# Kernel optimization log

Measured on AMD Instinct MI355X. Metric: run time of the kernel, lower is better.

The kernel has to match this reference:

```python
import jax, jax.numpy as jnp
import numpy as np

S = 128          # shared sequence length of v/q/a/k
D = 512          # model dim
H = 8            # n_heads
W = D // H       # head width (becomes the v/q/a einsum axes)
NUM = S // 8     # num_v = num_q = num_a = num_k
SCALE = float(np.sqrt(H))  # source divides by sqrt(a.size(-1)) == sqrt(n_heads)


def _heads(x):
    # split_last(x,(H,-1)).transpose(1,2) on a 2D (S,D) tensor -> (S, W, H)
    return x.reshape(S, H, W).transpose(0, 2, 1)


def setup_inputs() -> dict:
    key = jax.random.key(0)
    ks = jax.random.split(key, 24)
    d = {}
    for i, n in enumerate(['v', 'q', 'a', 'k']):
        d[n] = jax.random.normal(ks[i], (S, D), jnp.float32)
    for n in ['v_mask', 'q_mask', 'a_mask', 'k_mask']:
        d[n] = jnp.ones((S,), jnp.bool_)
    wnames = ['Wv', 'Wq', 'Wa', 'Wk', 'Wvo', 'Wqo', 'Wao', 'Wko']
    bnames = ['bv', 'bq', 'ba', 'bk', 'bvo', 'bqo', 'bao', 'bko']
    for i, (wn, bn) in enumerate(zip(wnames, bnames)):
        d[wn] = jax.random.normal(ks[4 + 2 * i], (D, D), jnp.float32) / np.sqrt(D)
        d[bn] = jax.random.normal(ks[5 + 2 * i], (D,), jnp.float32) * 0.01
    return d


def reference(v, q, a, k, v_mask, q_mask, a_mask, k_mask,
              Wv, bv, Wq, bq, Wa, ba, Wk, bk,
              Wvo, bvo, Wqo, bqo, Wao, bao, Wko, bko):
    # input projections (torch Linear: x @ W.T + b)
    vp = v @ Wv.T + bv
    qp = q @ Wq.T + bq
    ap = a @ Wa.T + ba
    kp = k @ Wk.T + bk
    # output projections are applied to the already-projected tensors
    vo = vp @ Wvo.T + bvo
    qo = qp @ Wqo.T + bqo
    ao = ap @ Wao.T + bao
    ko = kp @ Wko.T + bko
    tv, tq, ta, tk = map(_heads, (vp, qp, ap, kp))      # (S, W, H)
    tvo, tqo, tao, tko = map(_heads, (vo, qo, ao, ko))  # (S, W, H)
    # trilinear scores: in source labels b=1, h=S, v/q/a in W, w=H
    att = jnp.einsum('sic,sjc,slc->sijl', tv, tq, ta) / SCALE   # (S, W, W, W)
    att1 = jnp.einsum('sic,sjc,slc->sijl', tv, tq, tk) / SCALE  # (S, W, W, W)
    # joint softmax over the flat num_v*num_q*num_a axis (flat memory reshape,
    # exactly like torch .view); dropout p=0.0 -> identity
    scores = jax.nn.softmax(att.reshape(-1, H, NUM * NUM * NUM), axis=-1)
    scores = scores.reshape(-1, H, NUM, NUM, NUM)  # stored as self.scores in torch
    # output contractions use the UNNORMALIZED att1 (as in the source)
    v_res = jnp.einsum('sijl,sic->isc', att1, tvo).reshape(1, W, S * H)
    q_res = jnp.einsum('sijl,sjc->jsc', att1, tqo).reshape(1, W, S * H)
    a_res = jnp.einsum('sijl,slc->lsc', att1, tao).reshape(1, W, S * H)
    k_res = tko[None].reshape(1, S, W * H)
    return (v_res, q_res, a_res, k_res, scores)
```

## Files before the change

kernel.cpp:

```cpp
#include <hip/hip_runtime.h>
#include <hip/hip_bf16.h>

#define INV_SCALE 0.35355339059327373f

struct Proj4Args {
  const float* x[4];
  const float* w[4];
  const float* b[4];
  float* y[4];
};

__global__ __launch_bounds__(256) void proj4_kernel(Proj4Args A) {
  const int blk = blockIdx.x;
  const int p = blk >> 6;
  const int dbase = (blk & 63) * 8;
  const int t = threadIdx.x;
  const int s = t & 127;
  const int h = t >> 7;
  __shared__ float WL[8 * 512];
  __shared__ float XT[32][129];
  {
    const float4* wg = (const float4*)(A.w[p] + dbase * 512);
    float4* wl4 = (float4*)WL;
#pragma unroll
    for (int r = 0; r < 4; ++r) wl4[t + r * 256] = wg[t + r * 256];
  }
  const float* xg = A.x[p];
  const int row = t >> 3;
  const int col = t & 7;
  float acc[4] = {0.f, 0.f, 0.f, 0.f};
  float4 pre[4];
#pragma unroll
  for (int r = 0; r < 4; ++r)
    pre[r] = ((const float4*)(xg + (row + r * 32) * 512))[col];
  for (int c = 0; c < 16; ++c) {
    __syncthreads();
#pragma unroll
    for (int r = 0; r < 4; ++r) {
      float4 f = pre[r];
      int rr = row + r * 32;
      XT[col * 4 + 0][rr] = f.x;
      XT[col * 4 + 1][rr] = f.y;
      XT[col * 4 + 2][rr] = f.z;
      XT[col * 4 + 3][rr] = f.w;
    }
    __syncthreads();
    if (c + 1 < 16) {
#pragma unroll
      for (int r = 0; r < 4; ++r)
        pre[r] = ((const float4*)(xg + (row + r * 32) * 512))[(c + 1) * 8 + col];
    }
#pragma unroll
    for (int k4 = 0; k4 < 8; ++k4) {
      float xv0 = XT[k4 * 4 + 0][s];
      float xv1 = XT[k4 * 4 + 1][s];
      float xv2 = XT[k4 * 4 + 2][s];
      float xv3 = XT[k4 * 4 + 3][s];
#pragma unroll
      for (int di = 0; di < 4; ++di) {
        const float4 wv =
            *(const float4*)&WL[(h * 4 + di) * 512 + c * 32 + k4 * 4];
        acc[di] = fmaf(wv.x, xv0, acc[di]);
        acc[di] = fmaf(wv.y, xv1, acc[di]);
        acc[di] = fmaf(wv.z, xv2, acc[di]);
        acc[di] = fmaf(wv.w, xv3, acc[di]);
      }
    }
  }
  const float* bp = A.b[p];
  float4 o;
  o.x = acc[0] + bp[dbase + h * 4 + 0];
  o.y = acc[1] + bp[dbase + h * 4 + 1];
  o.z = acc[2] + bp[dbase + h * 4 + 2];
  o.w = acc[3] + bp[dbase + h * 4 + 3];
  *(float4*)(A.y[p] + s * 512 + dbase + h * 4) = o;
}

__global__ __launch_bounds__(256) void post_kernel(
    const float* __restrict__ vp, const float* __restrict__ qp,
    const float* __restrict__ kp, const float* __restrict__ vo,
    const float* __restrict__ qo, const float* __restrict__ ao,
    const float* __restrict__ ko, float* __restrict__ out) {
  const int s = blockIdx.x;
  const int t = threadIdx.x;
  const int wid = t >> 6;
  const int ln = t & 63;
  __shared__ float Ssum[3][8];
  const float* srcs[3] = {vp, qp, kp};
#pragma unroll
  for (int tt = 0; tt < 3; ++tt) {
    const float* r = srcs[tt] + s * 512;
    float a = r[wid * 64 + ln];
    float b = r[256 + wid * 64 + ln];
#pragma unroll
    for (int o = 32; o; o >>= 1) {
      a += __shfl_xor(a, o);
      b += __shfl_xor(b, o);
    }
    if (ln == 0) { Ssum[tt][wid] = a; Ssum[tt][wid + 4] = b; }
  }
  __syncthreads();
  if (wid == 3) {
    float tmp[8];
#pragma unroll
    for (int h = 0; h < 8; ++h)
      tmp[h] = ko[s * 512 + h * 64 + ln];
    float4* pp = reinterpret_cast<float4*>(out + 196608 + (s * 64 + ln) * 8);
    pp[0] = make_float4(tmp[0], tmp[1], tmp[2], tmp[3]);
    pp[1] = make_float4(tmp[4], tmp[5], tmp[6], tmp[7]);
  } else {
    const float* base = (wid == 0) ? vp : (wid == 1) ? qp : kp;
    const float* obase = (wid == 0) ? vo : (wid == 1) ? qo : ao;
    const int c0 = (wid == 0) ? 1 : 0;
    const int c1 = (wid == 2) ? 1 : 2;
    float A1 = 0.f;
#pragma unroll
    for (int c = 0; c < 8; ++c)
      A1 += base[s * 512 + c * 64 + ln] * (Ssum[c0][c] * Ssum[c1][c]);
    A1 *= INV_SCALE;
    float tmp[8];
#pragma unroll
    for (int c = 0; c < 8; ++c)
      tmp[c] = obase[s * 512 + c * 64 + ln] * A1;
    float4* pp = reinterpret_cast<float4*>(out + wid * 65536 + (ln * 128 + s) * 8);
    pp[0] = make_float4(tmp[0], tmp[1], tmp[2], tmp[3]);
    pp[1] = make_float4(tmp[4], tmp[5], tmp[6], tmp[7]);
  }
}

__global__ __launch_bounds__(256) void scores_kernel(
    const float* __restrict__ vp, const float* __restrict__ qp,
    const float* __restrict__ ap, float* __restrict__ out) {
  const int b = blockIdx.x;
  const int s = b >> 4;
  const int i0 = (b & 15) * 4;
  const int t = threadIdx.x;
  __shared__ float tqL[512];
  __shared__ float taL[512];
  __shared__ float uL[32];
  __shared__ float redM[4][4];
  __shared__ float redS[4][4];
  {
    const float* qr = qp + s * 512;
    const float* ar = ap + s * 512;
    tqL[t] = qr[t]; tqL[t + 256] = qr[t + 256];
    taL[t] = ar[t]; taL[t + 256] = ar[t + 256];
    if (t < 32) {
      int ii = t >> 3, c = t & 7;
      uL[t] = vp[s * 512 + c * 64 + i0 + ii] * INV_SCALE;
    }
  }
  __syncthreads();
  const int j0 = t >> 3;
  const int l0 = (t & 7) * 8;
  float acc[4][16];
#pragma unroll
  for (int ii = 0; ii < 4; ++ii)
#pragma unroll
    for (int x = 0; x < 16; ++x) acc[ii][x] = 0.f;
#pragma unroll
  for (int c = 0; c < 8; ++c) {
    float t0 = tqL[c * 64 + j0];
    float t1 = tqL[c * 64 + j0 + 32];
    float4 A0 = *reinterpret_cast<const float4*>(&taL[c * 64 + l0]);
    float4 A1v = *reinterpret_cast<const float4*>(&taL[c * 64 + l0 + 4]);
    float ta8[8] = {A0.x, A0.y, A0.z, A0.w, A1v.x, A1v.y, A1v.z, A1v.w};
#pragma unroll
    for (int ii = 0; ii < 4; ++ii) {
      float uv = uL[ii * 8 + c];
      float m0 = uv * t0;
      float m1 = uv * t1;
#pragma unroll
      for (int x = 0; x < 8; ++x) {
        acc[ii][x] = fmaf(m0, ta8[x], acc[ii][x]);
        acc[ii][8 + x] = fmaf(m1, ta8[x], acc[ii][8 + x]);
      }
    }
  }
  const int wid = t >> 6, ln = t & 63;
#pragma unroll
  for (int ii = 0; ii < 4; ++ii) {
    float m = acc[ii][0];
#pragma unroll
    for (int x = 1; x < 16; ++x) m = fmaxf(m, acc[ii][x]);
#pragma unroll
    for (int o = 32; o; o >>= 1) m = fmaxf(m, __shfl_xor(m, o));
    if (ln == 0) redM[ii][wid] = m;
  }
  __syncthreads();
#pragma unroll
  for (int ii = 0; ii < 4; ++ii) {
    float mf = fmaxf(fmaxf(redM[ii][0], redM[ii][1]),
                     fmaxf(redM[ii][2], redM[ii][3]));
    float sl = 0.f;
#pragma unroll
    for (int x = 0; x < 16; ++x) {
      float e = __expf(acc[ii][x] - mf);
      acc[ii][x] = e;
      sl += e;
    }
#pragma unroll
    for (int o = 32; o; o >>= 1) sl += __shfl_xor(sl, o);
    if (ln == 0) redS[ii][wid] = sl;
  }
  __syncthreads();
  const long sbase = 262144L + (long)s * 262144 + (long)i0 * 4096;
#pragma unroll
  for (int ii = 0; ii < 4; ++ii) {
    float tot = (redS[ii][0] + redS[ii][1]) + (redS[ii][2] + redS[ii][3]);
    float sc = 1.0f / tot;
#pragma unroll
    for (int jj = 0; jj < 2; ++jj) {
      float4* pp = reinterpret_cast<float4*>(
          out + sbase + ii * 4096 + (j0 + jj * 32) * 64 + l0);
      pp[0] = make_float4(acc[ii][jj * 8 + 0] * sc, acc[ii][jj * 8 + 1] * sc,
                          acc[ii][jj * 8 + 2] * sc, acc[ii][jj * 8 + 3] * sc);
      pp[1] = make_float4(acc[ii][jj * 8 + 4] * sc, acc[ii][jj * 8 + 5] * sc,
                          acc[ii][jj * 8 + 6] * sc, acc[ii][jj * 8 + 7] * sc);
    }
  }
}

extern "C" void kernel_launch(void* const* d_in, const int* in_sizes, int n_in,
                              void* d_out, int out_size, void* d_ws, size_t ws_size,
                              hipStream_t stream) {
  int wb = 8;
  if (n_in >= 5 && in_sizes[4] == 262144) wb = 4;
  const float* W[8];
  const float* B[8];
  for (int i = 0; i < 8; ++i) {
    W[i] = (const float*)d_in[wb + 2 * i];
    B[i] = (const float*)d_in[wb + 2 * i + 1];
  }
  float* ws = (float*)d_ws;
  float* vp = ws;
  float* qp = ws + 65536;
  float* ap = ws + 131072;
  float* kp = ws + 196608;
  float* vo = ws + 262144;
  float* qo = ws + 327680;
  float* ao = ws + 393216;
  float* ko = ws + 458752;
  float* out = (float*)d_out;

  Proj4Args a1;
  for (int i = 0; i < 4; ++i) {
    a1.x[i] = (const float*)d_in[i];
    a1.w[i] = W[i];
    a1.b[i] = B[i];
  }
  a1.y[0] = vp; a1.y[1] = qp; a1.y[2] = ap; a1.y[3] = kp;
  hipLaunchKernelGGL(proj4_kernel, dim3(256), dim3(256), 0, stream, a1);

  Proj4Args a2;
  a2.x[0] = vp; a2.x[1] = qp; a2.x[2] = ap; a2.x[3] = kp;
  for (int i = 0; i < 4; ++i) {
    a2.w[i] = W[4 + i];
    a2.b[i] = B[4 + i];
  }
  a2.y[0] = vo; a2.y[1] = qo; a2.y[2] = ao; a2.y[3] = ko;
  hipLaunchKernelGGL(proj4_kernel, dim3(256), dim3(256), 0, stream, a2);

  hipLaunchKernelGGL(post_kernel, dim3(128), dim3(256), 0, stream,
                     vp, qp, kp, vo, qo, ao, ko, out);
  hipLaunchKernelGGL(scores_kernel, dim3(2048), dim3(256), 0, stream,
                     vp, qp, ap, out);
}
```

Baseline: 245.2 us.

## Merge second projection and scores kernels into one heterogeneous launch

```diff
diff --git a/kernel.cpp b/kernel.cpp
--- a/kernel.cpp
+++ b/kernel.cpp
@@ -10,15 +10,14 @@
   float* y[4];
 };
 
-__global__ __launch_bounds__(256) void proj4_kernel(Proj4Args A) {
-  const int blk = blockIdx.x;
+__device__ __forceinline__ void proj_body(const Proj4Args& A, int blk, int t,
+                                          float* SH) {
   const int p = blk >> 6;
   const int dbase = (blk & 63) * 8;
-  const int t = threadIdx.x;
   const int s = t & 127;
   const int h = t >> 7;
-  __shared__ float WL[8 * 512];
-  __shared__ float XT[32][129];
+  float* WL = SH;
+  float(*XT)[129] = (float(*)[129])(SH + 4096);
   {
     const float4* wg = (const float4*)(A.w[p] + dbase * 512);
     float4* wl4 = (float4*)WL;
@@ -74,6 +73,121 @@
   o.z = acc[2] + bp[dbase + h * 4 + 2];
   o.w = acc[3] + bp[dbase + h * 4 + 3];
   *(float4*)(A.y[p] + s * 512 + dbase + h * 4) = o;
+}
+
+__global__ __launch_bounds__(256) void proj4_kernel(Proj4Args A) {
+  __shared__ float SH[8224];
+  proj_body(A, blockIdx.x, threadIdx.x, SH);
+}
+
+__device__ __forceinline__ void scores_body(const float* __restrict__ vp,
+                                            const float* __restrict__ qp,
+                                            const float* __restrict__ ap,
+                                            float* __restrict__ out, int b,
+                                            int t, float* SH) {
+  const int s = b >> 4;
+  const int i0 = (b & 15) * 4;
+  float* tqL = SH;
+  float* taL = SH + 512;
+  float* uL = SH + 1024;
+  float(*redM)[4] = (float(*)[4])(SH + 1056);
+  float(*redS)[4] = (float(*)[4])(SH + 1072);
+  {
+    const float* qr = qp + s * 512;
+    const float* ar = ap + s * 512;
+    tqL[t] = qr[t]; tqL[t + 256] = qr[t + 256];
+    taL[t] = ar[t]; taL[t + 256] = ar[t + 256];
+    if (t < 32) {
+      int ii = t >> 3, c = t & 7;
+      uL[t] = vp[s * 512 + c * 64 + i0 + ii] * INV_SCALE;
+    }
+  }
+  __syncthreads();
+  const int j0 = t >> 3;
+  const int l0 = (t & 7) * 8;
+  float acc[4][16];
+#pragma unroll
+  for (int ii = 0; ii < 4; ++ii)
+#pragma unroll
+    for (int x = 0; x < 16; ++x) acc[ii][x] = 0.f;
+#pragma unroll
+  for (int c = 0; c < 8; ++c) {
+    float t0 = tqL[c * 64 + j0];
+    float t1 = tqL[c * 64 + j0 + 32];
+    float4 A0 = *reinterpret_cast<const float4*>(&taL[c * 64 + l0]);
+    float4 A1v = *reinterpret_cast<const float4*>(&taL[c * 64 + l0 + 4]);
+    float ta8[8] = {A0.x, A0.y, A0.z, A0.w, A1v.x, A1v.y, A1v.z, A1v.w};
+#pragma unroll
+    for (int ii = 0; ii < 4; ++ii) {
+      float uv = uL[ii * 8 + c];
+      float m0 = uv * t0;
+      float m1 = uv * t1;
+#pragma unroll
+      for (int x = 0; x < 8; ++x) {
+        acc[ii][x] = fmaf(m0, ta8[x], acc[ii][x]);
+        acc[ii][8 + x] = fmaf(m1, ta8[x], acc[ii][8 + x]);
+      }
+    }
+  }
+  const int wid = t >> 6, ln = t & 63;
+#pragma unroll
+  for (int ii = 0; ii < 4; ++ii) {
+    float m = acc[ii][0];
+#pragma unroll
+    for (int x = 1; x < 16; ++x) m = fmaxf(m, acc[ii][x]);
+#pragma unroll
+    for (int o = 32; o; o >>= 1) m = fmaxf(m, __shfl_xor(m, o));
+    if (ln == 0) redM[ii][wid] = m;
+  }
+  __syncthreads();
+#pragma unroll
+  for (int ii = 0; ii < 4; ++ii) {
+    float mf = fmaxf(fmaxf(redM[ii][0], redM[ii][1]),
+                     fmaxf(redM[ii][2], redM[ii][3]));
+    float sl = 0.f;
+#pragma unroll
+    for (int x = 0; x < 16; ++x) {
+      float e = __expf(acc[ii][x] - mf);
+      acc[ii][x] = e;
+      sl += e;
+    }
+#pragma unroll
+    for (int o = 32; o; o >>= 1) sl += __shfl_xor(sl, o);
+    if (ln == 0) redS[ii][wid] = sl;
+  }
+  __syncthreads();
+  const long sbase = 262144L + (long)s * 262144 + (long)i0 * 4096;
+#pragma unroll
+  for (int ii = 0; ii < 4; ++ii) {
+    float tot = (redS[ii][0] + redS[ii][1]) + (redS[ii][2] + redS[ii][3]);
+    float sc = 1.0f / tot;
+#pragma unroll
+    for (int jj = 0; jj < 2; ++jj) {
+      float4* pp = reinterpret_cast<float4*>(
+          out + sbase + ii * 4096 + (j0 + jj * 32) * 64 + l0);
+      pp[0] = make_float4(acc[ii][jj * 8 + 0] * sc, acc[ii][jj * 8 + 1] * sc,
+                          acc[ii][jj * 8 + 2] * sc, acc[ii][jj * 8 + 3] * sc);
+      pp[1] = make_float4(acc[ii][jj * 8 + 4] * sc, acc[ii][jj * 8 + 5] * sc,
+                          acc[ii][jj * 8 + 6] * sc, acc[ii][jj * 8 + 7] * sc);
+    }
+  }
+}
+
+struct FusedArgs {
+  Proj4Args pj;
+  const float* vp;
+  const float* qp;
+  const float* ap;
+  float* out;
+};
+
+__global__ __launch_bounds__(256) void fused_kernel(FusedArgs F) {
+  __shared__ float SH[8224];
+  const int b = blockIdx.x;
+  if (b < 2048)
+    scores_body(F.vp, F.qp, F.ap, F.out, b, threadIdx.x, SH);
+  else
+    proj_body(F.pj, b - 2048, threadIdx.x, SH);
 }
 
 __global__ __launch_bounds__(256) void post_kernel(
@@ -128,99 +242,6 @@
   }
 }
 
-__global__ __launch_bounds__(256) void scores_kernel(
-    const float* __restrict__ vp, const float* __restrict__ qp,
-    const float* __restrict__ ap, float* __restrict__ out) {
-  const int b = blockIdx.x;
-  const int s = b >> 4;
-  const int i0 = (b & 15) * 4;
-  const int t = threadIdx.x;
-  __shared__ float tqL[512];
-  __shared__ float taL[512];
-  __shared__ float uL[32];
-  __shared__ float redM[4][4];
-  __shared__ float redS[4][4];
-  {
-    const float* qr = qp + s * 512;
-    const float* ar = ap + s * 512;
-    tqL[t] = qr[t]; tqL[t + 256] = qr[t + 256];
-    taL[t] = ar[t]; taL[t + 256] = ar[t + 256];
-    if (t < 32) {
-      int ii = t >> 3, c = t & 7;
-      uL[t] = vp[s * 512 + c * 64 + i0 + ii] * INV_SCALE;
-    }
-  }
-  __syncthreads();
-  const int j0 = t >> 3;
-  const int l0 = (t & 7) * 8;
-  float acc[4][16];
-#pragma unroll
-  for (int ii = 0; ii < 4; ++ii)
-#pragma unroll
-    for (int x = 0; x < 16; ++x) acc[ii][x] = 0.f;
-#pragma unroll
-  for (int c = 0; c < 8; ++c) {
-    float t0 = tqL[c * 64 + j0];
-    float t1 = tqL[c * 64 + j0 + 32];
-    float4 A0 = *reinterpret_cast<const float4*>(&taL[c * 64 + l0]);
-    float4 A1v = *reinterpret_cast<const float4*>(&taL[c * 64 + l0 + 4]);
-    float ta8[8] = {A0.x, A0.y, A0.z, A0.w, A1v.x, A1v.y, A1v.z, A1v.w};
-#pragma unroll
-    for (int ii = 0; ii < 4; ++ii) {
-      float uv = uL[ii * 8 + c];
-      float m0 = uv * t0;
-      float m1 = uv * t1;
-#pragma unroll
-      for (int x = 0; x < 8; ++x) {
-        acc[ii][x] = fmaf(m0, ta8[x], acc[ii][x]);
-        acc[ii][8 + x] = fmaf(m1, ta8[x], acc[ii][8 + x]);
-      }
-    }
-  }
-  const int wid = t >> 6, ln = t & 63;
-#pragma unroll
-  for (int ii = 0; ii < 4; ++ii) {
-    float m = acc[ii][0];
-#pragma unroll
-    for (int x = 1; x < 16; ++x) m = fmaxf(m, acc[ii][x]);
-#pragma unroll
-    for (int o = 32; o; o >>= 1) m = fmaxf(m, __shfl_xor(m, o));
-    if (ln == 0) redM[ii][wid] = m;
-  }
-  __syncthreads();
-#pragma unroll
-  for (int ii = 0; ii < 4; ++ii) {
-    float mf = fmaxf(fmaxf(redM[ii][0], redM[ii][1]),
-                     fmaxf(redM[ii][2], redM[ii][3]));
-    float sl = 0.f;
-#pragma unroll
-    for (int x = 0; x < 16; ++x) {
-      float e = __expf(acc[ii][x] - mf);
-      acc[ii][x] = e;
-      sl += e;
-    }
-#pragma unroll
-    for (int o = 32; o; o >>= 1) sl += __shfl_xor(sl, o);
-    if (ln == 0) redS[ii][wid] = sl;
-  }
-  __syncthreads();
-  const long sbase = 262144L + (long)s * 262144 + (long)i0 * 4096;
-#pragma unroll
-  for (int ii = 0; ii < 4; ++ii) {
-    float tot = (redS[ii][0] + redS[ii][1]) + (redS[ii][2] + redS[ii][3]);
-    float sc = 1.0f / tot;
-#pragma unroll
-    for (int jj = 0; jj < 2; ++jj) {
-      float4* pp = reinterpret_cast<float4*>(
-          out + sbase + ii * 4096 + (j0 + jj * 32) * 64 + l0);
-      pp[0] = make_float4(acc[ii][jj * 8 + 0] * sc, acc[ii][jj * 8 + 1] * sc,
-                          acc[ii][jj * 8 + 2] * sc, acc[ii][jj * 8 + 3] * sc);
-      pp[1] = make_float4(acc[ii][jj * 8 + 4] * sc, acc[ii][jj * 8 + 5] * sc,
-                          acc[ii][jj * 8 + 6] * sc, acc[ii][jj * 8 + 7] * sc);
-    }
-  }
-}
-
 extern "C" void kernel_launch(void* const* d_in, const int* in_sizes, int n_in,
                               void* d_out, int out_size, void* d_ws, size_t ws_size,
                               hipStream_t stream) {
@@ -252,17 +273,16 @@
   a1.y[0] = vp; a1.y[1] = qp; a1.y[2] = ap; a1.y[3] = kp;
   hipLaunchKernelGGL(proj4_kernel, dim3(256), dim3(256), 0, stream, a1);
 
-  Proj4Args a2;
-  a2.x[0] = vp; a2.x[1] = qp; a2.x[2] = ap; a2.x[3] = kp;
+  FusedArgs F;
+  F.pj.x[0] = vp; F.pj.x[1] = qp; F.pj.x[2] = ap; F.pj.x[3] = kp;
   for (int i = 0; i < 4; ++i) {
-    a2.w[i] = W[4 + i];
-    a2.b[i] = B[4 + i];
-  }
-  a2.y[0] = vo; a2.y[1] = qo; a2.y[2] = ao; a2.y[3] = ko;
-  hipLaunchKernelGGL(proj4_kernel, dim3(256), dim3(256), 0, stream, a2);
+    F.pj.w[i] = W[4 + i];
+    F.pj.b[i] = B[4 + i];
+  }
+  F.pj.y[0] = vo; F.pj.y[1] = qo; F.pj.y[2] = ao; F.pj.y[3] = ko;
+  F.vp = vp; F.qp = qp; F.ap = ap; F.out = out;
+  hipLaunchKernelGGL(fused_kernel, dim3(2304), dim3(256), 0, stream, F);
 
   hipLaunchKernelGGL(post_kernel, dim3(128), dim3(256), 0, stream,
                      vp, qp, kp, vo, qo, ao, ko, out);
-  hipLaunchKernelGGL(scores_kernel, dim3(2048), dim3(256), 0, stream,
-                     vp, qp, ap, out);
-}
+}
```

After: 240.1 us. -2.1%, faster.
